# Optimization experiments

Measured on AMD Instinct MI355X. Metric: run time of the kernel, lower is better.

## Reference

```python
import jax, jax.numpy as jnp
import numpy as np

N = 100000
D = 128


def segment_mean(x, idx, n):
    s = jax.ops.segment_sum(x, idx, num_segments=n)
    c = jax.ops.segment_sum(jnp.ones((idx.shape[0],), x.dtype), idx, num_segments=n)
    return s / jnp.maximum(c, 1.0)[:, None]


def setup_inputs() -> dict:
    key = jax.random.key(0)
    ks = jax.random.split(key, 10)
    scale = 1.0 / np.sqrt(D)
    return {
        "embedding": jax.random.normal(ks[0], (N, D), dtype=jnp.float32),
        "W_down": jax.random.normal(ks[1], (D, D), dtype=jnp.float32) * scale,
        "b_down": jnp.zeros((D,), dtype=jnp.float32),
        "W_gcn": jax.random.normal(ks[2], (D, D), dtype=jnp.float32) * scale,
        "b_gcn": jnp.zeros((D,), dtype=jnp.float32),
        "W_up": jax.random.normal(ks[3], (D, D), dtype=jnp.float32) * scale,
        "b_up": jnp.zeros((D,), dtype=jnp.float32),
        "down2up_path": jax.random.randint(ks[4], (2, 100000), 0, N),
        "same_level_edge_index": jax.random.randint(ks[5], (2, 600000), 0, N),
        "up2down_edge_index": jax.random.randint(ks[6], (2, 100000), 0, N),
    }


def _forward(embedding, W_down, b_down, W_gcn, b_gcn, W_up, b_up,
             down2up_path, same_level_edge_index, up2down_edge_index):
    # ---- Down2Up: aggregate children into parents (mean), transform, residual add ----
    src, dst = down2up_path[0], down2up_path[1]
    agg = segment_mean(embedding[src], dst, N)                     # [N, D]
    x = jax.nn.relu(embedding + agg @ W_down + b_down)

    # ---- Same-level GCNConv with self-loops and symmetric normalization ----
    s, d = same_level_edge_index[0], same_level_edge_index[1]
    h = x @ W_gcn                                                  # [N, D]
    deg = jax.ops.segment_sum(jnp.ones((s.shape[0],), h.dtype), d, num_segments=N) + 1.0
    dinv = jax.lax.rsqrt(deg)                                      # deg^{-1/2}
    norm = dinv[s] * dinv[d]                                       # [E]
    x = jax.ops.segment_sum(norm[:, None] * h[s], d, num_segments=N)
    x = x + h * (1.0 / deg)[:, None] + b_gcn                       # self-loop term

    # ---- Up2Down: propagate parents back down to children (mean), transform, residual ----
    src2, dst2 = up2down_edge_index[0], up2down_edge_index[1]
    agg2 = segment_mean(x[src2], dst2, N)
    return jax.nn.relu(x + agg2 @ W_up + b_up)


def reference(embedding, W_down, b_down, W_gcn, b_gcn, W_up, b_up,
              down2up_path, same_level_edge_index, up2down_edge_index):
    return _forward(embedding, W_down, b_down, W_gcn, b_gcn, W_up, b_up,
                    down2up_path, same_level_edge_index, up2down_edge_index)
```

## Files before the change

### kernel.cpp

```cpp
#include <hip/hip_runtime.h>
#include <cstdint>
#include <cstddef>

#define NNODES 100000
#define DIM 128
#define TLD 144

#define NB3   (3 * NNODES)
#define BSH   9
#define NBUCK ((NB3 + 511) >> 9)
#define EPB   2048

typedef unsigned short u16;
typedef uint32_t u32;
typedef __attribute__((ext_vector_type(8))) short v8s;
typedef __attribute__((ext_vector_type(4))) float v4f;

__device__ __forceinline__ float bf2f(u32 u) {
  union { u32 i; float f; } x; x.i = u << 16; return x.f;
}
__device__ __forceinline__ u16 f2bf(float f) {
  union { float f; u32 i; } x; x.f = f;
  u32 r = x.i + 0x7fffu + ((x.i >> 16) & 1u);
  return (u16)(r >> 16);
}
__device__ __forceinline__ u32 packsplit(float f) {
  u16 h = f2bf(f);
  float r = f - bf2f(h);
  u16 l = f2bf(r);
  return (u32)h | ((u32)l << 16);
}


__global__ __launch_bounds__(256) void bin_count(const int* __restrict__ d2u,
    const int* __restrict__ sle, const int* __restrict__ u2d,
    int E1, int E2, int E3, int* __restrict__ bcnt) {
  __shared__ int lc[NBUCK];
  const int tid = threadIdx.x;
  for (int i = tid; i < NBUCK; i += 256) lc[i] = 0;
  __syncthreads();
  const int Etot = E1 + E2 + E3;
  const int base = blockIdx.x * EPB;
#pragma unroll
  for (int k = 0; k < EPB; k += 256) {
    int e = base + k + tid;
    if (e < Etot) {
      int idx;
      if (e < E1)            idx = d2u[E1 + e];
      else if (e < E1 + E2)  idx = NNODES + sle[E2 + (e - E1)];
      else                   idx = 2 * NNODES + u2d[E3 + (e - E1 - E2)];
      atomicAdd(&lc[idx >> BSH], 1);
    }
  }
  __syncthreads();
  for (int i = tid; i < NBUCK; i += 256)
    if (lc[i]) atomicAdd(&bcnt[i], lc[i]);
}

__global__ void bin_scan(const int* __restrict__ bcnt, int* __restrict__ brs,
                         int* __restrict__ bfill) {
  __shared__ int tmp[1024];
  const int tid = threadIdx.x;
  for (int i = tid; i < 1024; i += 256) tmp[i] = (i < NBUCK) ? bcnt[i] : 0;
  __syncthreads();
  for (int off = 1; off < 1024; off <<= 1) {
    int vals[4];
#pragma unroll
    for (int j = 0; j < 4; ++j) { int i = tid + j * 256; vals[j] = (i >= off) ? tmp[i - off] : 0; }
    __syncthreads();
#pragma unroll
    for (int j = 0; j < 4; ++j) { int i = tid + j * 256; tmp[i] += vals[j]; }
    __syncthreads();
  }
  for (int i = tid; i < NBUCK; i += 256) {
    int excl = tmp[i] - bcnt[i];
    brs[i] = excl;
    bfill[i] = excl;
  }
}

__global__ __launch_bounds__(256) void bin_fill(const int* __restrict__ d2u,
    const int* __restrict__ sle, const int* __restrict__ u2d,
    int E1, int E2, int E3, int* __restrict__ bfill, uint2* __restrict__ pairs) {
  __shared__ int lc[NBUCK];
  const int tid = threadIdx.x;
  for (int i = tid; i < NBUCK; i += 256) lc[i] = 0;
  __syncthreads();
  const int Etot = E1 + E2 + E3;
  const int base = blockIdx.x * EPB;
  int vidx[EPB / 256], vsrc[EPB / 256];
#pragma unroll
  for (int k = 0; k < EPB / 256; ++k) {
    int e = base + k * 256 + tid;
    int idx = -1, src = 0;
    if (e < Etot) {
      if (e < E1)            { idx = d2u[E1 + e];                          src = d2u[e]; }
      else if (e < E1 + E2)  { int q = e - E1;      idx = NNODES + sle[E2 + q];      src = sle[q]; }
      else                   { int q = e - E1 - E2; idx = 2 * NNODES + u2d[E3 + q];  src = u2d[q]; }
      atomicAdd(&lc[idx >> BSH], 1);
    }
    vidx[k] = idx; vsrc[k] = src;
  }
  __syncthreads();
  for (int i = tid; i < NBUCK; i += 256) {
    int c = lc[i];
    if (c) lc[i] = atomicAdd(&bfill[i], c);
  }
  __syncthreads();
#pragma unroll
  for (int k = 0; k < EPB / 256; ++k) {
    int idx = vidx[k];
    if (idx >= 0) {
      int pos = atomicAdd(&lc[idx >> BSH], 1);
      pairs[pos] = make_uint2((unsigned)idx, (unsigned)vsrc[k]);
    }
  }
}

__global__ __launch_bounds__(256) void node_count(const uint2* __restrict__ pairs,
    const int* __restrict__ brs, const int* __restrict__ bcnt, int* __restrict__ cnt) {
  __shared__ int c[512];
  const int tid = threadIdx.x;
  const int b = blockIdx.x;
  for (int i = tid; i < 512; i += 256) c[i] = 0;
  __syncthreads();
  const int s = brs[b], m = bcnt[b];
  for (int k = tid; k < m; k += 256) {
    uint2 p = pairs[s + k];
    atomicAdd(&c[p.x & 511], 1);
  }
  __syncthreads();
  const int node0 = b << BSH;
  for (int i = tid; i < 512; i += 256) {
    int g = node0 + i;
    if (g < NB3) cnt[g] = c[i];
  }
}

__global__ __launch_bounds__(256) void scatter_bucket(const uint2* __restrict__ pairs,
    const int* __restrict__ brs, const int* __restrict__ bcnt,
    const int* __restrict__ rs, int* __restrict__ eidx) {
  __shared__ int cur[512];
  const int tid = threadIdx.x;
  const int b = blockIdx.x;
  const int node0 = b << BSH;
  for (int i = tid; i < 512; i += 256) {
    int g = node0 + i;
    cur[i] = (g < NB3) ? rs[g] : 0;
  }
  __syncthreads();
  const int s = brs[b], m = bcnt[b];
  for (int k = tid; k < m; k += 256) {
    uint2 p = pairs[s + k];
    int pos = atomicAdd(&cur[p.x & 511], 1);
    eidx[pos] = (int)p.y;
  }
}


__global__ void scan_blocks(const int* __restrict__ in, int* __restrict__ out,
                            int* __restrict__ bsum, int n) {
  __shared__ int wsum[4];
  const int tid = threadIdx.x;
  const int base = blockIdx.x * 1024 + tid * 4;
  int v0 = 0, v1 = 0, v2 = 0, v3 = 0;
  if (base + 0 < n) v0 = in[base + 0];
  if (base + 1 < n) v1 = in[base + 1];
  if (base + 2 < n) v2 = in[base + 2];
  if (base + 3 < n) v3 = in[base + 3];
  const int tsum = v0 + v1 + v2 + v3;
  const int lane = tid & 63, wid = tid >> 6;
  int x = tsum;
  for (int off = 1; off < 64; off <<= 1) {
    int y = __shfl_up(x, off, 64);
    if (lane >= off) x += y;
  }
  if (lane == 63) wsum[wid] = x;
  __syncthreads();
  int woff = 0;
  for (int w = 0; w < wid; ++w) woff += wsum[w];
  const int excl = woff + x - tsum;
  if (base + 0 < n) out[base + 0] = excl;
  if (base + 1 < n) out[base + 1] = excl + v0;
  if (base + 2 < n) out[base + 2] = excl + v0 + v1;
  if (base + 3 < n) out[base + 3] = excl + v0 + v1 + v2;
  if (tid == 255) bsum[blockIdx.x] = woff + x;
}

__global__ void scan_top(int* __restrict__ bsum, int nb) {
  __shared__ int tmp[1024];
  const int tid = threadIdx.x;
  for (int i = tid; i < 1024; i += 256) tmp[i] = (i < nb) ? bsum[i] : 0;
  __syncthreads();
  for (int off = 1; off < 1024; off <<= 1) {
    int vals[4];
#pragma unroll
    for (int j = 0; j < 4; ++j) { int i = tid + j * 256; vals[j] = (i >= off) ? tmp[i - off] : 0; }
    __syncthreads();
#pragma unroll
    for (int j = 0; j < 4; ++j) { int i = tid + j * 256; tmp[i] += vals[j]; }
    __syncthreads();
  }
  for (int i = tid; i < nb; i += 256) {
    int orig = bsum[i];
    bsum[i] = tmp[i] - orig;
  }
}

__global__ void scan_add(int* __restrict__ out, const int* __restrict__ bsum, int n) {
  const int b = blockIdx.x;
  const int off = bsum[b];
  const int base = b * 1024 + threadIdx.x * 4;
#pragma unroll
  for (int j = 0; j < 4; ++j)
    if (base + j < n) out[base + j] += off;
}

__global__ void make_rnorm(const int* __restrict__ cntB, float* __restrict__ rnorm, int n) {
  int i = blockIdx.x * 256 + threadIdx.x;
  if (i < n) rnorm[i] = rsqrtf((float)cntB[i] + 1.0f);
}

__global__ void make_w_planes(const float* __restrict__ W0, const float* __restrict__ W1,
                              const float* __restrict__ W2,
                              u16* __restrict__ Whi, u16* __restrict__ Wlo) {
  int i = blockIdx.x * 256 + threadIdx.x;
  if (i >= 3 * DIM * DIM) return;
  int j = i & 7, lane = (i >> 3) & 63, ct = (i >> 9) & 7, kk = (i >> 12) & 3, m = i >> 14;
  int lr = lane & 15, quad = lane >> 4;
  int c = ct * 16 + lr;
  int k = kk * 32 + quad * 8 + j;
  const float* W = (m == 0) ? W0 : ((m == 1) ? W1 : W2);
  u32 p = packsplit(W[k * DIM + c]);
  Whi[i] = (u16)(p & 0xffffu);
  Wlo[i] = (u16)(p >> 16);
}


__global__ void gather_gcn(const u16* __restrict__ g,
                           const int* __restrict__ rs, const int* __restrict__ cnt,
                           const int* __restrict__ eidx, const float* __restrict__ rnorm,
                           const float* __restrict__ bias, float* __restrict__ out, int n) {
  int gid = blockIdx.x * 256 + threadIdx.x;
  int i = gid >> 6;
  if (i >= n) return;
  int sub = gid & 63;
  int c = (sub & 31) << 2;
  int start = rs[i], m = cnt[i];
  float4 acc = {0.f, 0.f, 0.f, 0.f};
  if (sub < 32) {
    ushort4 pv = *(const ushort4*)(g + ((size_t)i << 7) + c);
    acc.x = bf2f(pv.x); acc.y = bf2f(pv.y);
    acc.z = bf2f(pv.z); acc.w = bf2f(pv.w);
  }
  int j = sub >> 5;
  for (; j + 2 < m; j += 4) {
    int s0 = eidx[start + j], s1 = eidx[start + j + 2];
    ushort4 p0 = *(const ushort4*)(g + ((size_t)s0 << 7) + c);
    ushort4 p1 = *(const ushort4*)(g + ((size_t)s1 << 7) + c);
    acc.x += bf2f(p0.x) + bf2f(p1.x);
    acc.y += bf2f(p0.y) + bf2f(p1.y);
    acc.z += bf2f(p0.z) + bf2f(p1.z);
    acc.w += bf2f(p0.w) + bf2f(p1.w);
  }
  if (j < m) {
    int s = eidx[start + j];
    ushort4 pv = *(const ushort4*)(g + ((size_t)s << 7) + c);
    acc.x += bf2f(pv.x); acc.y += bf2f(pv.y);
    acc.z += bf2f(pv.z); acc.w += bf2f(pv.w);
  }
  acc.x += __shfl_xor(acc.x, 32);
  acc.y += __shfl_xor(acc.y, 32);
  acc.z += __shfl_xor(acc.z, 32);
  acc.w += __shfl_xor(acc.w, 32);
  if (sub < 32) {
    float ri = rnorm[i];
    float4 bv = *(const float4*)(bias + c);
    float4 o;
    o.x = fmaf(ri, acc.x, bv.x);
    o.y = fmaf(ri, acc.y, bv.y);
    o.z = fmaf(ri, acc.z, bv.z);
    o.w = fmaf(ri, acc.w, bv.w);
    *(float4*)(out + (size_t)i * DIM + c) = o;
  }
}

__global__ __launch_bounds__(512) void fused_ab(
    const float* __restrict__ emb,
    const int* __restrict__ rs, const int* __restrict__ cnt, const int* __restrict__ eidx,
    const u16* __restrict__ Wdh, const u16* __restrict__ Wdl,
    const u16* __restrict__ Wgh, const u16* __restrict__ Wgl,
    const float* __restrict__ bd, const float* __restrict__ rnorm,
    u16* __restrict__ obf, int nrows)
{
  __shared__ u16 S[2 * DIM * DIM];
  u32* X = (u32*)S;
  const int tid = threadIdx.x;
  const int wave = tid >> 6, lane = tid & 63;
  const int lr = lane & 15, quad = lane >> 4;
  const int rowbase = blockIdx.x * 128 + wave * 16;

  int arow = rowbase + lr;
  if (arow >= nrows) arow = nrows - 1;
  const int start = rs[arow], m = cnt[arow];
  float4 fa[4], fb[4];
#pragma unroll
  for (int kk = 0; kk < 4; ++kk) {
    fa[kk] = (float4){0.f, 0.f, 0.f, 0.f};
    fb[kk] = (float4){0.f, 0.f, 0.f, 0.f};
  }
  for (int j = 0; j < m; ++j) {
    int s = eidx[start + j];
    const float* rp = emb + (size_t)s * DIM + quad * 8;
#pragma unroll
    for (int kk = 0; kk < 4; ++kk) {
      float4 v0 = *(const float4*)(rp + kk * 32);
      float4 v1 = *(const float4*)(rp + kk * 32 + 4);
      fa[kk].x += v0.x; fa[kk].y += v0.y; fa[kk].z += v0.z; fa[kk].w += v0.w;
      fb[kk].x += v1.x; fb[kk].y += v1.y; fb[kk].z += v1.z; fb[kk].w += v1.w;
    }
  }
  const float inv = 1.0f / fmaxf((float)m, 1.0f);
  v8s afh[4], afl[4];
#pragma unroll
  for (int kk = 0; kk < 4; ++kk) {
    float vs[8] = {fa[kk].x, fa[kk].y, fa[kk].z, fa[kk].w,
                   fb[kk].x, fb[kk].y, fb[kk].z, fb[kk].w};
#pragma unroll
    for (int j = 0; j < 8; ++j) {
      u32 p = packsplit(vs[j] * inv);
      afh[kk][j] = (short)(p & 0xffffu);
      afl[kk][j] = (short)(p >> 16);
    }
  }

  {
    uint4* W4 = (uint4*)S;
    for (int i = tid; i < DIM * DIM / 8; i += 512)
      W4[i] = ((const uint4*)Wdh)[i];
  }
  __syncthreads();

  v4f acc[8];
#pragma unroll
  for (int ct = 0; ct < 8; ++ct) acc[ct] = (v4f){0.f, 0.f, 0.f, 0.f};
#pragma unroll
  for (int kk = 0; kk < 4; ++kk) {
#pragma unroll
    for (int ct = 0; ct < 8; ++ct) {
      const int wo = ((kk * 8 + ct) << 9) + (lane << 3);
      v8s bh = *(const v8s*)(S + wo);
      v8s bl = *(const v8s*)(Wdl + wo);
      acc[ct] = __builtin_amdgcn_mfma_f32_16x16x32_bf16(afh[kk], bh, acc[ct], 0, 0, 0);
      acc[ct] = __builtin_amdgcn_mfma_f32_16x16x32_bf16(afh[kk], bl, acc[ct], 0, 0, 0);
      acc[ct] = __builtin_amdgcn_mfma_f32_16x16x32_bf16(afl[kk], bh, acc[ct], 0, 0, 0);
    }
  }

  __syncthreads();

#pragma unroll
  for (int rg = 0; rg < 4; ++rg) {
    int r = rowbase + quad * 4 + rg;
    int rc = (r < nrows) ? r : (nrows - 1);
#pragma unroll
    for (int ct = 0; ct < 8; ++ct) {
      const int col = ct * 16 + lr;
      float v = acc[ct][rg] + bd[col] + emb[(size_t)rc * DIM + col];
      v = fmaxf(v, 0.f);
      X[wave * 2048 + (((rg << 3) + ct) << 6) + (quad << 4) + lr] = packsplit(v);
    }
  }

  v8s agh[4], agl[4];
#pragma unroll
  for (int kk = 0; kk < 4; ++kk) {
    const int base = wave * 2048 + ((((lr & 3) << 3) + kk * 2 + (quad >> 1)) << 6) +
                     (((lr >> 2) & 3) << 4) + ((quad & 1) << 3);
    uint4 q0 = *(const uint4*)(X + base);
    uint4 q1 = *(const uint4*)(X + base + 4);
    u32 u[8] = {q0.x, q0.y, q0.z, q0.w, q1.x, q1.y, q1.z, q1.w};
#pragma unroll
    for (int j = 0; j < 8; ++j) {
      agh[kk][j] = (short)(u[j] & 0xffffu);
      agl[kk][j] = (short)(u[j] >> 16);
    }
  }

#pragma unroll
  for (int ct = 0; ct < 8; ++ct) acc[ct] = (v4f){0.f, 0.f, 0.f, 0.f};
#pragma unroll
  for (int kk = 0; kk < 4; ++kk) {
#pragma unroll
    for (int ct = 0; ct < 8; ++ct) {
      const int wo = ((kk * 8 + ct) << 9) + (lane << 3);
      v8s bh = *(const v8s*)(Wgh + wo);
      v8s bl = *(const v8s*)(Wgl + wo);
      acc[ct] = __builtin_amdgcn_mfma_f32_16x16x32_bf16(agh[kk], bh, acc[ct], 0, 0, 0);
      acc[ct] = __builtin_amdgcn_mfma_f32_16x16x32_bf16(agh[kk], bl, acc[ct], 0, 0, 0);
      acc[ct] = __builtin_amdgcn_mfma_f32_16x16x32_bf16(agl[kk], bh, acc[ct], 0, 0, 0);
    }
  }

  __syncthreads();

  const int lrow0 = wave * 16 + quad * 4;
#pragma unroll
  for (int rg = 0; rg < 4; ++rg) {
    int lrow = lrow0 + rg;
    int r = blockIdx.x * 128 + lrow;
    float sc = rnorm[(r < nrows) ? r : (nrows - 1)];
#pragma unroll
    for (int ct = 0; ct < 8; ++ct) {
      S[lrow * TLD + ct * 16 + lr] = f2bf(acc[ct][rg] * sc);
    }
  }
  __syncthreads();
  const int rowstart = blockIdx.x * 128;
  for (int idx = tid; idx < 128 * 16; idx += 512) {
    int lrow = idx >> 4, c8 = (idx & 15) << 3;
    int r = rowstart + lrow;
    if (r < nrows)
      *(uint4*)(obf + ((size_t)r << 7) + c8) = *(const uint4*)&S[lrow * TLD + c8];
  }
}

__global__ __launch_bounds__(512) void gather_gemm_c(
    const float* __restrict__ x,
    const int* __restrict__ rs, const int* __restrict__ cnt, const int* __restrict__ eidx,
    const u16* __restrict__ Wuh, const u16* __restrict__ Wul,
    const float* __restrict__ bias, float* __restrict__ outf, int nrows)
{
  __shared__ u16 Wh[DIM * DIM];
  const int tid = threadIdx.x;
  const int wave = tid >> 6, lane = tid & 63;
  const int lr = lane & 15, quad = lane >> 4;
  const int rowbase = blockIdx.x * 128 + wave * 16;

  int arow = rowbase + lr;
  if (arow >= nrows) arow = nrows - 1;
  const int start = rs[arow], m = cnt[arow];
  float4 fa[4], fb[4];
#pragma unroll
  for (int kk = 0; kk < 4; ++kk) {
    fa[kk] = (float4){0.f, 0.f, 0.f, 0.f};
    fb[kk] = (float4){0.f, 0.f, 0.f, 0.f};
  }
  for (int j = 0; j < m; ++j) {
    int s = eidx[start + j];
    const float* rp = x + (size_t)s * DIM + quad * 8;
#pragma unroll
    for (int kk = 0; kk < 4; ++kk) {
      float4 v0 = *(const float4*)(rp + kk * 32);
      float4 v1 = *(const float4*)(rp + kk * 32 + 4);
      fa[kk].x += v0.x; fa[kk].y += v0.y; fa[kk].z += v0.z; fa[kk].w += v0.w;
      fb[kk].x += v1.x; fb[kk].y += v1.y; fb[kk].z += v1.z; fb[kk].w += v1.w;
    }
  }
  const float inv = 1.0f / fmaxf((float)m, 1.0f);
  v8s afh[4], afl[4];
#pragma unroll
  for (int kk = 0; kk < 4; ++kk) {
    float vs[8] = {fa[kk].x, fa[kk].y, fa[kk].z, fa[kk].w,
                   fb[kk].x, fb[kk].y, fb[kk].z, fb[kk].w};
#pragma unroll
    for (int j = 0; j < 8; ++j) {
      u32 p = packsplit(vs[j] * inv);
      afh[kk][j] = (short)(p & 0xffffu);
      afl[kk][j] = (short)(p >> 16);
    }
  }

  {
    uint4* W4 = (uint4*)Wh;
    for (int i = tid; i < DIM * DIM / 8; i += 512)
      W4[i] = ((const uint4*)Wuh)[i];
  }
  __syncthreads();

  v4f acc[8];
#pragma unroll
  for (int ct = 0; ct < 8; ++ct) acc[ct] = (v4f){0.f, 0.f, 0.f, 0.f};
#pragma unroll
  for (int kk = 0; kk < 4; ++kk) {
#pragma unroll
    for (int ct = 0; ct < 8; ++ct) {
      const int wo = ((kk * 8 + ct) << 9) + (lane << 3);
      v8s bh = *(const v8s*)(Wh + wo);
      v8s bl = *(const v8s*)(Wul + wo);
      acc[ct] = __builtin_amdgcn_mfma_f32_16x16x32_bf16(afh[kk], bh, acc[ct], 0, 0, 0);
      acc[ct] = __builtin_amdgcn_mfma_f32_16x16x32_bf16(afh[kk], bl, acc[ct], 0, 0, 0);
      acc[ct] = __builtin_amdgcn_mfma_f32_16x16x32_bf16(afl[kk], bh, acc[ct], 0, 0, 0);
    }
  }

#pragma unroll
  for (int ct = 0; ct < 8; ++ct) {
    const int col = ct * 16 + lr;
    float bv = bias[col];
#pragma unroll
    for (int rg = 0; rg < 4; ++rg) {
      int r = rowbase + quad * 4 + rg;
      if (r < nrows) {
        size_t off = (size_t)r * DIM + col;
        float v = acc[ct][rg] + bv + x[off];
        outf[off] = fmaxf(v, 0.f);
      }
    }
  }
}


extern "C" void kernel_launch(void* const* d_in, const int* in_sizes, int n_in,
                              void* d_out, int out_size, void* d_ws, size_t ws_size,
                              hipStream_t stream) {
  const float* emb = (const float*)d_in[0];
  const float* Wd  = (const float*)d_in[1];
  const float* bd  = (const float*)d_in[2];
  const float* Wg  = (const float*)d_in[3];
  const float* bg  = (const float*)d_in[4];
  const float* Wu  = (const float*)d_in[5];
  const float* bu  = (const float*)d_in[6];
  const int* d2u = (const int*)d_in[7];
  const int* sle = (const int*)d_in[8];
  const int* u2d = (const int*)d_in[9];
  const int E1 = in_sizes[7] / 2;
  const int E2 = in_sizes[8] / 2;
  const int E3 = in_sizes[9] / 2;
  const int Etot = E1 + E2 + E3;
  const int N  = NNODES;
  const size_t nd = (size_t)N * DIM;

  float* xb = (float*)d_ws;
  u16* Gbf  = (u16*)(xb + nd);
  int* cnt  = (int*)(Gbf + nd);
  int* bbuf = cnt + 3 * N;
  int* rs   = bbuf + 3 * 1024;
  int* eidx = rs + 3 * N;
  float* rnorm = (float*)(eidx + Etot);
  int* bsum = (int*)(rnorm + N);
  u16* Whi = (u16*)(bsum + 1024);
  u16* Wlo = Whi + 3 * DIM * DIM;
  uint2* pairs = (uint2*)(Wlo + 3 * DIM * DIM);
  int* bcnt  = bbuf;
  int* brs   = bbuf + 1024;
  int* bfill = bbuf + 2048;

  const int gemm_blocks = (N + 127) / 128;
  const int nscan = (3 * N + 1023) / 1024;
  const int ngcn = (N * 64 + 255) / 256;
  const int nbin = (Etot + EPB - 1) / EPB;

  (void)hipMemsetAsync(bcnt, 0, 1024 * sizeof(int), stream);
  make_w_planes<<<(3 * DIM * DIM + 255) / 256, 256, 0, stream>>>(Wd, Wg, Wu, Whi, Wlo);
  bin_count<<<nbin, 256, 0, stream>>>(d2u, sle, u2d, E1, E2, E3, bcnt);
  bin_scan<<<1, 256, 0, stream>>>(bcnt, brs, bfill);
  bin_fill<<<nbin, 256, 0, stream>>>(d2u, sle, u2d, E1, E2, E3, bfill, pairs);
  node_count<<<NBUCK, 256, 0, stream>>>(pairs, brs, bcnt, cnt);
  make_rnorm<<<(N + 255) / 256, 256, 0, stream>>>(cnt + N, rnorm, N);
  scan_blocks<<<nscan, 256, 0, stream>>>(cnt, rs, bsum, 3 * N);
  scan_top<<<1, 256, 0, stream>>>(bsum, nscan);
  scan_add<<<nscan, 256, 0, stream>>>(rs, bsum, 3 * N);
  scatter_bucket<<<NBUCK, 256, 0, stream>>>(pairs, brs, bcnt, rs, eidx);

  fused_ab<<<gemm_blocks, 512, 0, stream>>>(emb, rs, cnt, eidx,
                                            Whi, Wlo, Whi + DIM * DIM, Wlo + DIM * DIM,
                                            bd, rnorm, Gbf, N);

  gather_gcn<<<ngcn, 256, 0, stream>>>(Gbf, rs + N, cnt + N, eidx, rnorm, bg, xb, N);

  gather_gemm_c<<<gemm_blocks, 512, 0, stream>>>(xb, rs + 2 * N, cnt + 2 * N, eidx,
                                                 Whi + 2 * DIM * DIM, Wlo + 2 * DIM * DIM,
                                                 bu, (float*)d_out, N);
}
```

Before: 309.7 us.

## Stage low-half weights in LDS and stream GEMM1 output into GEMM2 per K-slice

The low-half bf16 weights (Wdl, Wul) are now staged in LDS alongside the high halves instead of being read from global memory inside the MFMA loops. The fused kernel writes the first GEMM's activations into a small XOR-swizzled per-wave staging area two column tiles at a time, interleaved with the second GEMM's K-slices, so only one 16-wide K chunk of A fragments is held at a time. This cuts global weight traffic, reduces register pressure from the four-chunk A fragment arrays, and avoids LDS bank conflicts. In exchange there is more LDS per block (64KB in each kernel) and a second accumulator array live across the loop, which could limit occupancy.

New measurement: 291.3 us. 5.9% less time.

```diff
diff --git a/kernel.cpp b/kernel.cpp
--- a/kernel.cpp
+++ b/kernel.cpp
@@ -293,8 +293,8 @@
     const float* __restrict__ bd, const float* __restrict__ rnorm,
     u16* __restrict__ obf, int nrows)
 {
-  __shared__ u16 S[2 * DIM * DIM];
-  u32* X = (u32*)S;
+  __shared__ u16 S[32768];
+  u32* X = (u32*)(S + 16384);
   const int tid = threadIdx.x;
   const int wave = tid >> 6, lane = tid & 63;
   const int lr = lane & 15, quad = lane >> 4;
@@ -335,9 +335,11 @@
   }
 
   {
-    uint4* W4 = (uint4*)S;
-    for (int i = tid; i < DIM * DIM / 8; i += 512)
-      W4[i] = ((const uint4*)Wdh)[i];
+    uint4* S4 = (uint4*)S;
+    for (int i = tid; i < 2048; i += 512) {
+      S4[i] = ((const uint4*)Wdh)[i];
+      S4[2048 + i] = ((const uint4*)Wdl)[i];
+    }
   }
   __syncthreads();
 
@@ -350,55 +352,81 @@
     for (int ct = 0; ct < 8; ++ct) {
       const int wo = ((kk * 8 + ct) << 9) + (lane << 3);
       v8s bh = *(const v8s*)(S + wo);
-      v8s bl = *(const v8s*)(Wdl + wo);
+      v8s bl = *(const v8s*)(S + 16384 + wo);
       acc[ct] = __builtin_amdgcn_mfma_f32_16x16x32_bf16(afh[kk], bh, acc[ct], 0, 0, 0);
       acc[ct] = __builtin_amdgcn_mfma_f32_16x16x32_bf16(afh[kk], bl, acc[ct], 0, 0, 0);
       acc[ct] = __builtin_amdgcn_mfma_f32_16x16x32_bf16(afl[kk], bh, acc[ct], 0, 0, 0);
     }
   }
-
-  __syncthreads();
-
-#pragma unroll
-  for (int rg = 0; rg < 4; ++rg) {
-    int r = rowbase + quad * 4 + rg;
-    int rc = (r < nrows) ? r : (nrows - 1);
+  __syncthreads();
+
+  {
+    uint4* S4 = (uint4*)S;
+    for (int i = tid; i < 2048; i += 512)
+      S4[i] = ((const uint4*)Wgh)[i];
+  }
+
+#pragma unroll
+  for (int cl = 0; cl < 2; ++cl) {
+#pragma unroll
+    for (int rg = 0; rg < 4; ++rg) {
+      int r = rowbase + quad * 4 + rg;
+      int rc = (r < nrows) ? r : (nrows - 1);
+      const int col = cl * 16 + lr;
+      float v = acc[cl][rg] + bd[col] + emb[(size_t)rc * DIM + col];
+      v = fmaxf(v, 0.f);
+      int slot = ((rg << 1) | cl) * 64 + (quad << 4) + lr;
+      slot ^= ((slot >> 6) & 7) << 2;
+      X[wave * 512 + slot] = packsplit(v);
+    }
+  }
+  __syncthreads();
+
+  v4f acc2[8];
+#pragma unroll
+  for (int ct = 0; ct < 8; ++ct) acc2[ct] = (v4f){0.f, 0.f, 0.f, 0.f};
+#pragma unroll
+  for (int Q = 0; Q < 4; ++Q) {
+    v8s agh, agl;
+    {
+      int s0 = ((lr & 3) * 2 + (quad >> 1)) * 64 + ((lr >> 2) << 4) + ((quad & 1) << 3);
+      int s1 = s0 + 4;
+      s0 ^= ((s0 >> 6) & 7) << 2;
+      s1 ^= ((s1 >> 6) & 7) << 2;
+      uint4 q0 = *(const uint4*)(X + wave * 512 + s0);
+      uint4 q1 = *(const uint4*)(X + wave * 512 + s1);
+      u32 u[8] = {q0.x, q0.y, q0.z, q0.w, q1.x, q1.y, q1.z, q1.w};
+#pragma unroll
+      for (int j = 0; j < 8; ++j) {
+        agh[j] = (short)(u[j] & 0xffffu);
+        agl[j] = (short)(u[j] >> 16);
+      }
+    }
 #pragma unroll
     for (int ct = 0; ct < 8; ++ct) {
-      const int col = ct * 16 + lr;
-      float v = acc[ct][rg] + bd[col] + emb[(size_t)rc * DIM + col];
-      v = fmaxf(v, 0.f);
-      X[wave * 2048 + (((rg << 3) + ct) << 6) + (quad << 4) + lr] = packsplit(v);
-    }
-  }
-
-  v8s agh[4], agl[4];
-#pragma unroll
-  for (int kk = 0; kk < 4; ++kk) {
-    const int base = wave * 2048 + ((((lr & 3) << 3) + kk * 2 + (quad >> 1)) << 6) +
-                     (((lr >> 2) & 3) << 4) + ((quad & 1) << 3);
-    uint4 q0 = *(const uint4*)(X + base);
-    uint4 q1 = *(const uint4*)(X + base + 4);
-    u32 u[8] = {q0.x, q0.y, q0.z, q0.w, q1.x, q1.y, q1.z, q1.w};
-#pragma unroll
-    for (int j = 0; j < 8; ++j) {
-      agh[kk][j] = (short)(u[j] & 0xffffu);
-      agl[kk][j] = (short)(u[j] >> 16);
-    }
-  }
-
-#pragma unroll
-  for (int ct = 0; ct < 8; ++ct) acc[ct] = (v4f){0.f, 0.f, 0.f, 0.f};
-#pragma unroll
-  for (int kk = 0; kk < 4; ++kk) {
-#pragma unroll
-    for (int ct = 0; ct < 8; ++ct) {
-      const int wo = ((kk * 8 + ct) << 9) + (lane << 3);
-      v8s bh = *(const v8s*)(Wgh + wo);
+      const int wo = ((Q * 8 + ct) << 9) + (lane << 3);
+      v8s bh = *(const v8s*)(S + wo);
       v8s bl = *(const v8s*)(Wgl + wo);
-      acc[ct] = __builtin_amdgcn_mfma_f32_16x16x32_bf16(agh[kk], bh, acc[ct], 0, 0, 0);
-      acc[ct] = __builtin_amdgcn_mfma_f32_16x16x32_bf16(agh[kk], bl, acc[ct], 0, 0, 0);
-      acc[ct] = __builtin_amdgcn_mfma_f32_16x16x32_bf16(agl[kk], bh, acc[ct], 0, 0, 0);
+      acc2[ct] = __builtin_amdgcn_mfma_f32_16x16x32_bf16(agh, bh, acc2[ct], 0, 0, 0);
+      acc2[ct] = __builtin_amdgcn_mfma_f32_16x16x32_bf16(agh, bl, acc2[ct], 0, 0, 0);
+      acc2[ct] = __builtin_amdgcn_mfma_f32_16x16x32_bf16(agl, bh, acc2[ct], 0, 0, 0);
+    }
+    if (Q < 3) {
+#pragma unroll
+      for (int cl = 0; cl < 2; ++cl) {
+        int ct = 2 * (Q + 1) + cl;
+#pragma unroll
+        for (int rg = 0; rg < 4; ++rg) {
+          int r = rowbase + quad * 4 + rg;
+          int rc = (r < nrows) ? r : (nrows - 1);
+          const int col = ct * 16 + lr;
+          float v = acc[ct][rg] + bd[col] + emb[(size_t)rc * DIM + col];
+          v = fmaxf(v, 0.f);
+          int slot = ((rg << 1) | cl) * 64 + (quad << 4) + lr;
+          slot ^= ((slot >> 6) & 7) << 2;
+          X[wave * 512 + slot] = packsplit(v);
+        }
+      }
     }
   }
 
@@ -412,7 +440,7 @@
     float sc = rnorm[(r < nrows) ? r : (nrows - 1)];
 #pragma unroll
     for (int ct = 0; ct < 8; ++ct) {
-      S[lrow * TLD + ct * 16 + lr] = f2bf(acc[ct][rg] * sc);
+      S[lrow * TLD + ct * 16 + lr] = f2bf(acc2[ct][rg] * sc);
     }
   }
   __syncthreads();
@@ -431,7 +459,7 @@
     const u16* __restrict__ Wuh, const u16* __restrict__ Wul,
     const float* __restrict__ bias, float* __restrict__ outf, int nrows)
 {
-  __shared__ u16 Wh[DIM * DIM];
+  __shared__ u16 W[2 * DIM * DIM];
   const int tid = threadIdx.x;
   const int wave = tid >> 6, lane = tid & 63;
   const int lr = lane & 15, quad = lane >> 4;
@@ -472,9 +500,11 @@
   }
 
   {
-    uint4* W4 = (uint4*)Wh;
-    for (int i = tid; i < DIM * DIM / 8; i += 512)
+    uint4* W4 = (uint4*)W;
+    for (int i = tid; i < 2048; i += 512) {
       W4[i] = ((const uint4*)Wuh)[i];
+      W4[2048 + i] = ((const uint4*)Wul)[i];
+    }
   }
   __syncthreads();
 
@@ -486,8 +516,8 @@
 #pragma unroll
     for (int ct = 0; ct < 8; ++ct) {
       const int wo = ((kk * 8 + ct) << 9) + (lane << 3);
-      v8s bh = *(const v8s*)(Wh + wo);
-      v8s bl = *(const v8s*)(Wul + wo);
+      v8s bh = *(const v8s*)(W + wo);
+      v8s bl = *(const v8s*)(W + DIM * DIM + wo);
       acc[ct] = __builtin_amdgcn_mfma_f32_16x16x32_bf16(afh[kk], bh, acc[ct], 0, 0, 0);
       acc[ct] = __builtin_amdgcn_mfma_f32_16x16x32_bf16(afh[kk], bl, acc[ct], 0, 0, 0);
       acc[ct] = __builtin_amdgcn_mfma_f32_16x16x32_bf16(afl[kk], bh, acc[ct], 0, 0, 0);
```
